# Kernel optimization log

Hardware: AMD Instinct MI355X
Metric: run time of the kernel (lower is better)

The kernel has to match this reference:

```python
import jax, jax.numpy as jnp
import numpy as np

N_STEPS = 64          # sample['N']
G = 1.0               # sample['g'] (constant diffusion)
NUM_SAMPLES = 2       # num_samples_per_obs
W_SCALE = 0.05

# interpolant coefficients: alpha(s)=1-s, beta(s)=s, sigma(s)=1-s
# derivatives: alpha_dot=-1, beta_dot=1, sigma_dot=-1

def b_net(x, x0, s, W1, b1, W2, b2, W3, b3):
    # B_net(interpolant, current_state, s): MLP on concat([x, x0, s])
    sf = jnp.full(x.shape[:-1] + (1,), s, dtype=x.dtype)
    inp = jnp.concatenate([x, x0, sf], axis=-1)      # [B, 2*dim+1]
    h = jax.nn.relu(inp @ W1 + b1)
    h = jax.nn.relu(h @ W2 + b2)
    return h @ W3 + b3                                # [B, dim]


def setup_inputs() -> dict:
    key = jax.random.key(0)
    ks = jax.random.split(key, 4)
    num_obs, dim, hid = 65536, 64, 256
    X0 = jax.random.normal(ks[0], (num_obs, dim), dtype=jnp.float32)
    W1 = jax.random.normal(ks[1], (2 * dim + 1, hid), dtype=jnp.float32) * W_SCALE
    W2 = jax.random.normal(ks[2], (hid, hid), dtype=jnp.float32) * W_SCALE
    W3 = jax.random.normal(ks[3], (hid, dim), dtype=jnp.float32) * W_SCALE
    return {
        "X0": X0,
        "W1": W1, "b1": jnp.zeros((hid,), jnp.float32),
        "W2": W2, "b2": jnp.zeros((hid,), jnp.float32),
        "W3": W3, "b3": jnp.zeros((dim,), jnp.float32),
    }


def reference(X0, W1, b1, W2, b2, W3, b3):
    time = jnp.linspace(0.0, 1.0, N_STEPS + 1, dtype=X0.dtype)
    ds = jnp.asarray(1.0 / N_STEPS, X0.dtype)
    sqrt_ds = jnp.sqrt(ds)
    params = (W1, b1, W2, b2, W3, b3)

    def sample_one(key):
        k0, kloop = jax.random.split(key)
        # first Euler step: X = X0 + ds*B(X0,X0,0) + sigma(0)*sqrt(ds)*eta
        eta0 = jax.random.normal(k0, X0.shape, X0.dtype)
        X = X0 + ds * b_net(X0, X0, time[0], *params) + (1.0 - time[0]) * sqrt_ds * eta0

        def step(carry, n):
            X, key = carry
            key, kn = jax.random.split(key)
            s = time[n]
            al, ald = 1.0 - s, -1.0
            bt, btd = s, 1.0
            sg, sgd = 1.0 - s, -1.0
            drift_b = b_net(X, X0, s, *params)
            # score correction (self.score)
            c = btd * X + (bt * ald - btd * al) * X0
            A = 1.0 / (s * sg * (btd * sg - bt * sgd))
            score = A * (bt * drift_b - c)
            # adjusted drift: drift + 0.5*(g^2 - sigma^2)*score
            control = 0.5 * (G ** 2 - sg ** 2) * score
            eta = jax.random.normal(kn, X.shape, X.dtype)
            X = X + ds * (drift_b + control) + G * sqrt_ds * eta
            return (X, key), None

        (X, _), _ = jax.lax.scan(step, (X, kloop), jnp.arange(1, N_STEPS))
        return X

    keys = jax.random.split(jax.random.key(1), NUM_SAMPLES)
    samples = jax.vmap(sample_one)(keys)   # [num_samples, num_obs, dim]
    return samples
```

## Files before the change

### kernel.cpp

```cpp
#include <hip/hip_runtime.h>
#include <stdint.h>


#define PARTITIONABLE 1

namespace {

constexpr int   kObs    = 65536;
constexpr int   kDim    = 64;
constexpr int   kSteps  = 64;
constexpr float kDs     = 1.0f / 64.0f;
constexpr float kSqrtDs = 0.125f;

constexpr int kWeightBytes = 256 * 1024;
constexpr int kKeysOff     = kWeightBytes;
constexpr int kStabOff     = kKeysOff + 1024;

typedef _Float16 f16x8 __attribute__((ext_vector_type(8)));
typedef _Float16 f16x4 __attribute__((ext_vector_type(4)));
typedef float    f32x4 __attribute__((ext_vector_type(4)));

#define MFMA16(a, b, c) __builtin_amdgcn_mfma_f32_16x16x32_f16((a), (b), (c), 0, 0, 0)

__device__ __forceinline__ uint32_t rotl(uint32_t v, int r) {
  return (v << r) | (v >> (32 - r));
}

__device__ __forceinline__ void tf2x32(uint32_t k0, uint32_t k1,
                                       uint32_t& x0, uint32_t& x1) {
  uint32_t k2 = k0 ^ k1 ^ 0x1BD11BDAu;
  x0 += k0; x1 += k1;
  x0 += x1; x1 = rotl(x1, 13); x1 ^= x0;
  x0 += x1; x1 = rotl(x1, 15); x1 ^= x0;
  x0 += x1; x1 = rotl(x1, 26); x1 ^= x0;
  x0 += x1; x1 = rotl(x1,  6); x1 ^= x0;
  x0 += k1; x1 += k2 + 1u;
  x0 += x1; x1 = rotl(x1, 17); x1 ^= x0;
  x0 += x1; x1 = rotl(x1, 29); x1 ^= x0;
  x0 += x1; x1 = rotl(x1, 16); x1 ^= x0;
  x0 += x1; x1 = rotl(x1, 24); x1 ^= x0;
  x0 += k2; x1 += k0 + 2u;
  x0 += x1; x1 = rotl(x1, 13); x1 ^= x0;
  x0 += x1; x1 = rotl(x1, 15); x1 ^= x0;
  x0 += x1; x1 = rotl(x1, 26); x1 ^= x0;
  x0 += x1; x1 = rotl(x1,  6); x1 ^= x0;
  x0 += k0; x1 += k1 + 3u;
  x0 += x1; x1 = rotl(x1, 17); x1 ^= x0;
  x0 += x1; x1 = rotl(x1, 29); x1 ^= x0;
  x0 += x1; x1 = rotl(x1, 16); x1 ^= x0;
  x0 += x1; x1 = rotl(x1, 24); x1 ^= x0;
  x0 += k1; x1 += k2 + 4u;
  x0 += x1; x1 = rotl(x1, 13); x1 ^= x0;
  x0 += x1; x1 = rotl(x1, 15); x1 ^= x0;
  x0 += x1; x1 = rotl(x1, 26); x1 ^= x0;
  x0 += x1; x1 = rotl(x1,  6); x1 ^= x0;
  x0 += k2; x1 += k0 + 5u;
}

__device__ __forceinline__ void jax_split(uint32_t k0, uint32_t k1,
                                          uint32_t& a0, uint32_t& a1,
                                          uint32_t& b0, uint32_t& b1) {
#if PARTITIONABLE
  uint32_t x0 = 0u, x1 = 0u; tf2x32(k0, k1, x0, x1); a0 = x0; a1 = x1;
  uint32_t y0 = 0u, y1 = 1u; tf2x32(k0, k1, y0, y1); b0 = y0; b1 = y1;
#else
  uint32_t x0 = 0u, x1 = 2u; tf2x32(k0, k1, x0, x1);
  uint32_t y0 = 1u, y1 = 3u; tf2x32(k0, k1, y0, y1);
  a0 = x0; a1 = y0; b0 = x1; b1 = y1;
#endif
}

__device__ __forceinline__ uint32_t draw_bits(uint32_t k0, uint32_t k1, uint32_t i) {
#if PARTITIONABLE
  uint32_t x0 = 0u, x1 = i;
  tf2x32(k0, k1, x0, x1);
  return x0 ^ x1;
#else
  const uint32_t half = (uint32_t)kObs * kDim / 2;
  if (i < half) {
    uint32_t x0 = i, x1 = i + half; tf2x32(k0, k1, x0, x1); return x0;
  } else {
    uint32_t x0 = i - half, x1 = i; tf2x32(k0, k1, x0, x1); return x1;
  }
#endif
}

__device__ __forceinline__ float erfinv32(float x) {
  float w = -__logf(fmaf(-x, x, 1.0f));
  float p;
  if (w < 5.0f) {
    w = w - 2.5f;
    p =            2.81022636e-08f;
    p = fmaf(p, w, 3.43273939e-07f);
    p = fmaf(p, w, -3.5233877e-06f);
    p = fmaf(p, w, -4.39150654e-06f);
    p = fmaf(p, w, 0.00021858087f);
    p = fmaf(p, w, -0.00125372503f);
    p = fmaf(p, w, -0.00417768164f);
    p = fmaf(p, w, 0.246640727f);
    p = fmaf(p, w, 1.50140941f);
  } else {
    w = sqrtf(w) - 3.0f;
    p =            -0.000200214257f;
    p = fmaf(p, w, 0.000100950558f);
    p = fmaf(p, w, 0.00134934322f);
    p = fmaf(p, w, -0.00367342844f);
    p = fmaf(p, w, 0.00573950773f);
    p = fmaf(p, w, -0.0076224613f);
    p = fmaf(p, w, 0.00943887047f);
    p = fmaf(p, w, 1.00167406f);
    p = fmaf(p, w, 2.83297682f);
  }
  return p * x;
}

__device__ __forceinline__ float bits_to_normal(uint32_t bits) {
  const float lo = -0.99999994f;
  float f = __uint_as_float(0x3f800000u | (bits >> 9)) - 1.0f;
  float u = fmaxf(lo, fmaf(f, 2.0f, lo));
  return 1.41421356237f * erfinv32(u);
}

}

__global__ void prep_weights(const float* __restrict__ W1,
                             const float* __restrict__ W2,
                             const float* __restrict__ W3,
                             _Float16* __restrict__ ws) {
  const int G = blockIdx.x;
  const int t = threadIdx.x;

  if (G >= 256) {
    if (t < 2) {
      uint32_t* kout = (uint32_t*)((char*)ws + kKeysOff) + t * 128;
      uint32_t s0a, s0b, s1a, s1b;
      jax_split(0u, 1u, s0a, s0b, s1a, s1b);
      const uint32_t sk0 = t ? s1a : s0a;
      const uint32_t sk1 = t ? s1b : s0b;
      uint32_t kd0, kd1, kl0, kl1;
      jax_split(sk0, sk1, kd0, kd1, kl0, kl1);
      kout[0] = kd0; kout[1] = kd1;
      for (int n = 1; n < kSteps; ++n) {
        uint32_t na, nb, xa, xb;
        jax_split(kl0, kl1, na, nb, xa, xb);
        kl0 = na; kl1 = nb;
        kout[2 * n] = xa; kout[2 * n + 1] = xb;
      }
    }
    if (t < kSteps) {
      const float s  = (float)t * kDs;
      const float sg = 1.0f - s;
      f32x4 v;
      v[0] = s;
      v[1] = (t == 0) ? 0.0f : 1.0f / (s * sg);
      v[2] = 0.5f * (1.0f - sg * sg);
      v[3] = 0.0f;
      *(f32x4*)((char*)ws + kStabOff + t * 16) = v;
    }
    return;
  }

  const int lane = t >> 2;
  const int j0   = (t & 3) * 2;
  const int w    = G >> 5;
  const int T    = G & 31;
  const int lm   = lane & 15;
  const int kb   = (lane >> 4) << 3;

#pragma unroll
  for (int jj = 0; jj < 2; ++jj) {
    const int j = j0 + jj;
    float v;
    if (T < 8) {
      const int mt = T >> 2, kt = T & 3;
      const int col = w * 32 + mt * 16 + lm;
      const int k   = kt * 32 + kb + j;
      v = W1[k * 256 + col];
    } else if (T < 24) {
      const int u = T - 8;
      const int mt = u >> 3, kt = u & 7;
      const int col = w * 32 + mt * 16 + lm;
      const int k   = kt * 32 + kb + j;
      v = W2[k * 256 + col];
    } else {
      const int kt  = T - 24;
      const int col = (w >> 1) * 16 + lm;
      const int k   = kt * 32 + kb + j;
      v = W3[k * 64 + col];
    }
    ws[(size_t)G * 512 + lane * 8 + j] = (_Float16)v;
  }
}

__global__ __launch_bounds__(512, 2)
void sde_mfma(const float* __restrict__ X0g,
              const float* __restrict__ W1,
              const float* __restrict__ b1,
              const float* __restrict__ b2,
              const float* __restrict__ b3,
              const _Float16* __restrict__ ws,
              float* __restrict__ out) {
  __shared__ alignas(16) _Float16 xA [64][72];
  __shared__ alignas(16) _Float16 x0A[64][72];
  __shared__ alignas(16) _Float16 h1 [64][264];
  __shared__ alignas(16) _Float16 h2 [64][264];
  __shared__ alignas(16) float    bb [832];

  const int t    = threadIdx.x;
  const int w    = t >> 6;
  const int l    = t & 63;
  const int lq   = l >> 4;
  const int lm   = l & 15;
  const int samp = blockIdx.x >> 10;
  const int tile = blockIdx.x & 1023;
  const int r0   = tile * 64;
  const int mt3  = w >> 1;
  const int ntb  = (w & 1) * 2;
  const int d0   = mt3 * 16 + lq * 4;

  if (t < 256) {
    bb[t]       = b1[t];
    bb[256 + t] = W1[128 * 256 + t];
    bb[512 + t] = b2[t];
  } else if (t < 320) {
    bb[768 + (t - 256)] = b3[t - 256];
  }

  {
    const int li = t >> 3;
    const int ci = (t & 7) * 8;
    const float* p = X0g + (size_t)(r0 + li) * kDim + ci;
    const float4 a = *(const float4*)p;
    const float4 b = *(const float4*)(p + 4);
    f16x8 h;
    h[0] = (_Float16)a.x; h[1] = (_Float16)a.y;
    h[2] = (_Float16)a.z; h[3] = (_Float16)a.w;
    h[4] = (_Float16)b.x; h[5] = (_Float16)b.y;
    h[6] = (_Float16)b.z; h[7] = (_Float16)b.w;
    *(f16x8*)&xA [li][ci] = h;
    *(f16x8*)&x0A[li][ci] = h;
  }

  float xv[2][4];
  f32x4 x0q[2];
#pragma unroll
  for (int ni = 0; ni < 2; ++ni) {
    const int row = (ntb + ni) * 16 + lm;
    x0q[ni] = *(const f32x4*)(X0g + (size_t)(r0 + row) * kDim + d0);
#pragma unroll
    for (int q = 0; q < 4; ++q) xv[ni][q] = x0q[ni][q];
  }

  f16x8 wreg[32];
  {
    const char* pW = (const char*)ws + (size_t)w * 32768 + l * 16;
#pragma unroll
    for (int i = 0; i < 32; ++i)
      wreg[i] = *(const f16x8*)(pW + i * 1024);
  }

  const uint32_t* keys = (const uint32_t*)((const char*)ws + kKeysOff) + samp * 128;
  const f32x4*    stab = (const f32x4*)((const char*)ws + kStabOff);

  __syncthreads();

  for (int n = 0; n < kSteps; ++n) {
    const f32x4 st = stab[n];
    const float s = st[0], A = st[1], coef = st[2];
    const uint32_t ka = keys[2 * n], kbk = keys[2 * n + 1];

#pragma unroll
    for (int nt = 0; nt < 4; ++nt) {
      const int row = nt * 16 + lm;
      f16x8 bf[4];
      bf[0] = *(const f16x8*)&xA [row][lq * 8];
      bf[1] = *(const f16x8*)&xA [row][32 + lq * 8];
      bf[2] = *(const f16x8*)&x0A[row][lq * 8];
      bf[3] = *(const f16x8*)&x0A[row][32 + lq * 8];
#pragma unroll
      for (int mt = 0; mt < 2; ++mt) {
        f32x4 c = {0.f, 0.f, 0.f, 0.f};
#pragma unroll
        for (int kt = 0; kt < 4; ++kt)
          c = MFMA16(wreg[mt * 4 + kt], bf[kt], c);
        const int nb = w * 32 + mt * 16 + lq * 4;
        const f32x4 bq = *(const f32x4*)&bb[nb];
        const f32x4 wq = *(const f32x4*)&bb[256 + nb];
        f16x4 o;
#pragma unroll
        for (int q = 0; q < 4; ++q)
          o[q] = (_Float16)fmaxf(c[q] + fmaf(s, wq[q], bq[q]), 0.f);
        *(f16x4*)&h1[row][nb] = o;
      }
    }
    __syncthreads();

#pragma unroll
    for (int ntp = 0; ntp < 2; ++ntp) {
      f32x4 c[2][2];
#pragma unroll
      for (int mt = 0; mt < 2; ++mt)
#pragma unroll
        for (int ni = 0; ni < 2; ++ni)
          c[mt][ni] = (f32x4){0.f, 0.f, 0.f, 0.f};
#pragma unroll
      for (int half = 0; half < 2; ++half) {
        f16x8 bh[2][4];
#pragma unroll
        for (int ni = 0; ni < 2; ++ni)
#pragma unroll
          for (int k4 = 0; k4 < 4; ++k4)
            bh[ni][k4] = *(const f16x8*)
                &h1[(ntp * 2 + ni) * 16 + lm][(half * 4 + k4) * 32 + lq * 8];
#pragma unroll
        for (int mt = 0; mt < 2; ++mt)
#pragma unroll
          for (int k4 = 0; k4 < 4; ++k4) {
            const f16x8 aW = wreg[8 + mt * 8 + half * 4 + k4];
            c[mt][0] = MFMA16(aW, bh[0][k4], c[mt][0]);
            c[mt][1] = MFMA16(aW, bh[1][k4], c[mt][1]);
          }
      }
#pragma unroll
      for (int mt = 0; mt < 2; ++mt) {
        const int nb = w * 32 + mt * 16 + lq * 4;
        const f32x4 bq = *(const f32x4*)&bb[512 + nb];
#pragma unroll
        for (int ni = 0; ni < 2; ++ni) {
          f16x4 o;
#pragma unroll
          for (int q = 0; q < 4; ++q)
            o[q] = (_Float16)fmaxf(c[mt][ni][q] + bq[q], 0.f);
          *(f16x4*)&h2[(ntp * 2 + ni) * 16 + lm][nb] = o;
        }
      }
    }
    __syncthreads();

    const f32x4 b3q = *(const f32x4*)&bb[768 + d0];
#pragma unroll
    for (int ni = 0; ni < 2; ++ni) {
      const int row = (ntb + ni) * 16 + lm;
      f32x4 dA = {0.f, 0.f, 0.f, 0.f}, dB = {0.f, 0.f, 0.f, 0.f};
#pragma unroll
      for (int half = 0; half < 2; ++half) {
        f16x8 bh[4];
#pragma unroll
        for (int k4 = 0; k4 < 4; ++k4)
          bh[k4] = *(const f16x8*)&h2[row][(half * 4 + k4) * 32 + lq * 8];
        dA = MFMA16(wreg[24 + half * 4 + 0], bh[0], dA);
        dB = MFMA16(wreg[24 + half * 4 + 1], bh[1], dB);
        dA = MFMA16(wreg[24 + half * 4 + 2], bh[2], dA);
        dB = MFMA16(wreg[24 + half * 4 + 3], bh[3], dB);
      }
      const uint32_t gi0 = (uint32_t)((r0 + row) * kDim + d0);
      f16x4 hx;
#pragma unroll
      for (int q = 0; q < 4; ++q) {
        const float ov    = dA[q] + dB[q] + b3q[q];
        const float eta   = bits_to_normal(draw_bits(ka, kbk, gi0 + q));
        const float score = A * (s * ov - (xv[ni][q] - x0q[ni][q]));
        const float nx    = xv[ni][q] + kDs * (ov + coef * score) + kSqrtDs * eta;
        xv[ni][q] = nx;
        hx[q] = (_Float16)nx;
      }
      *(f16x4*)&xA[row][d0] = hx;
    }
    __syncthreads();
  }

#pragma unroll
  for (int ni = 0; ni < 2; ++ni) {
    const int row = (ntb + ni) * 16 + lm;
    const size_t ob = (size_t)samp * ((size_t)kObs * kDim) +
                      (size_t)(r0 + row) * kDim + d0;
    f32x4 v;
#pragma unroll
    for (int q = 0; q < 4; ++q) v[q] = xv[ni][q];
    *(f32x4*)(out + ob) = v;
  }
}

extern "C" void kernel_launch(void* const* d_in, const int* in_sizes, int n_in,
                              void* d_out, int out_size, void* d_ws, size_t ws_size,
                              hipStream_t stream) {
  const float* X0 = (const float*)d_in[0];
  const float* W1 = (const float*)d_in[1];
  const float* b1 = (const float*)d_in[2];
  const float* W2 = (const float*)d_in[3];
  const float* b2 = (const float*)d_in[4];
  const float* W3 = (const float*)d_in[5];
  const float* b3 = (const float*)d_in[6];
  _Float16* ws = (_Float16*)d_ws;

  prep_weights<<<dim3(257), dim3(256), 0, stream>>>(W1, W2, W3, ws);
  sde_mfma<<<dim3(2048), dim3(512), 0, stream>>>(X0, W1, b1, b2, b3, ws,
                                                 (float*)d_out);
}
```

Measured before the change: 3.076 ms.

## Store LDS activations in MFMA-fragment order and hoist noise generation earlier

Replaces the padded row-major LDS arrays for x, x0, h1 and h2 with a fragment-tiled layout. In this layout each lane's MFMA operand is one contiguous 16-byte chunk at lane*16 within a 1 KB tile, which is meant to make LDS reads conflict-free and simpler to address. The Gaussian noise for the step is also computed earlier: the first half before layer 1 and the second half before the barrier that precedes layer 3. This lets the ALU-heavy RNG overlap with MFMA work instead of sitting on the critical tail. In exchange the index math is more intricate, and the precomputed noise values raise register pressure.

```diff
diff --git a/kernel.cpp b/kernel.cpp
--- a/kernel.cpp
+++ b/kernel.cpp
@@ -200,11 +200,11 @@
               const float* __restrict__ b3,
               const _Float16* __restrict__ ws,
               float* __restrict__ out) {
-  __shared__ alignas(16) _Float16 xA [64][72];
-  __shared__ alignas(16) _Float16 x0A[64][72];
-  __shared__ alignas(16) _Float16 h1 [64][264];
-  __shared__ alignas(16) _Float16 h2 [64][264];
-  __shared__ alignas(16) float    bb [832];
+  __shared__ alignas(16) char  xAf [8 * 1024];
+  __shared__ alignas(16) char  x0Af[8 * 1024];
+  __shared__ alignas(16) char  h1f [32 * 1024];
+  __shared__ alignas(16) char  h2f [32 * 1024];
+  __shared__ alignas(16) float bb  [832];
 
   const int t    = threadIdx.x;
   const int w    = t >> 6;
@@ -218,6 +218,11 @@
   const int ntb  = (w & 1) * 2;
   const int d0   = mt3 * 16 + lq * 4;
 
+  const int rb  = l * 16;
+  const int lo1 = ((lq >> 1) * 16 + lm) * 16 + (lq & 1) * 8;
+  const int kt3 = mt3 >> 1;
+  const int ln3 = (((mt3 & 1) * 2 + (lq >> 1)) * 16 + lm) * 16 + (lq & 1) * 8;
+
   if (t < 256) {
     bb[t]       = b1[t];
     bb[256 + t] = W1[128 * 256 + t];
@@ -237,8 +242,10 @@
     h[2] = (_Float16)a.z; h[3] = (_Float16)a.w;
     h[4] = (_Float16)b.x; h[5] = (_Float16)b.y;
     h[6] = (_Float16)b.z; h[7] = (_Float16)b.w;
-    *(f16x8*)&xA [li][ci] = h;
-    *(f16x8*)&x0A[li][ci] = h;
+    const int fa = ((ci >> 5) * 4 + (li >> 4)) * 1024 +
+                   (((ci >> 3) & 3) * 16 + (li & 15)) * 16;
+    *(f16x8*)(xAf  + fa) = h;
+    *(f16x8*)(x0Af + fa) = h;
   }
 
   float xv[2][4];
@@ -250,6 +257,8 @@
 #pragma unroll
     for (int q = 0; q < 4; ++q) xv[ni][q] = x0q[ni][q];
   }
+  const uint32_t giA = (uint32_t)((r0 + ntb * 16 + lm) * kDim + d0);
+  const uint32_t giB = giA + 16u * kDim;
 
   f16x8 wreg[32];
   {
@@ -269,14 +278,18 @@
     const float s = st[0], A = st[1], coef = st[2];
     const uint32_t ka = keys[2 * n], kbk = keys[2 * n + 1];
 
+    float etaA[4];
+#pragma unroll
+    for (int q = 0; q < 4; ++q)
+      etaA[q] = bits_to_normal(draw_bits(ka, kbk, giA + q));
+
 #pragma unroll
     for (int nt = 0; nt < 4; ++nt) {
-      const int row = nt * 16 + lm;
       f16x8 bf[4];
-      bf[0] = *(const f16x8*)&xA [row][lq * 8];
-      bf[1] = *(const f16x8*)&xA [row][32 + lq * 8];
-      bf[2] = *(const f16x8*)&x0A[row][lq * 8];
-      bf[3] = *(const f16x8*)&x0A[row][32 + lq * 8];
+      bf[0] = *(const f16x8*)(xAf  + (0 * 4 + nt) * 1024 + rb);
+      bf[1] = *(const f16x8*)(xAf  + (1 * 4 + nt) * 1024 + rb);
+      bf[2] = *(const f16x8*)(x0Af + (0 * 4 + nt) * 1024 + rb);
+      bf[3] = *(const f16x8*)(x0Af + (1 * 4 + nt) * 1024 + rb);
 #pragma unroll
       for (int mt = 0; mt < 2; ++mt) {
         f32x4 c = {0.f, 0.f, 0.f, 0.f};
@@ -290,7 +303,7 @@
 #pragma unroll
         for (int q = 0; q < 4; ++q)
           o[q] = (_Float16)fmaxf(c[q] + fmaf(s, wq[q], bq[q]), 0.f);
-        *(f16x4*)&h1[row][nb] = o;
+        *(f16x4*)(h1f + (w * 4 + nt) * 1024 + mt * 512 + lo1) = o;
       }
     }
     __syncthreads();
@@ -311,7 +324,7 @@
 #pragma unroll
           for (int k4 = 0; k4 < 4; ++k4)
             bh[ni][k4] = *(const f16x8*)
-                &h1[(ntp * 2 + ni) * 16 + lm][(half * 4 + k4) * 32 + lq * 8];
+                (h1f + ((half * 4 + k4) * 4 + ntp * 2 + ni) * 1024 + rb);
 #pragma unroll
         for (int mt = 0; mt < 2; ++mt)
 #pragma unroll
@@ -331,40 +344,44 @@
 #pragma unroll
           for (int q = 0; q < 4; ++q)
             o[q] = (_Float16)fmaxf(c[mt][ni][q] + bq[q], 0.f);
-          *(f16x4*)&h2[(ntp * 2 + ni) * 16 + lm][nb] = o;
+          *(f16x4*)(h2f + (w * 4 + ntp * 2 + ni) * 1024 + mt * 512 + lo1) = o;
         }
       }
     }
+
+    float etaB[4];
+#pragma unroll
+    for (int q = 0; q < 4; ++q)
+      etaB[q] = bits_to_normal(draw_bits(ka, kbk, giB + q));
     __syncthreads();
 
     const f32x4 b3q = *(const f32x4*)&bb[768 + d0];
 #pragma unroll
     for (int ni = 0; ni < 2; ++ni) {
-      const int row = (ntb + ni) * 16 + lm;
       f32x4 dA = {0.f, 0.f, 0.f, 0.f}, dB = {0.f, 0.f, 0.f, 0.f};
 #pragma unroll
       for (int half = 0; half < 2; ++half) {
         f16x8 bh[4];
 #pragma unroll
         for (int k4 = 0; k4 < 4; ++k4)
-          bh[k4] = *(const f16x8*)&h2[row][(half * 4 + k4) * 32 + lq * 8];
+          bh[k4] = *(const f16x8*)
+              (h2f + ((half * 4 + k4) * 4 + ntb + ni) * 1024 + rb);
         dA = MFMA16(wreg[24 + half * 4 + 0], bh[0], dA);
         dB = MFMA16(wreg[24 + half * 4 + 1], bh[1], dB);
         dA = MFMA16(wreg[24 + half * 4 + 2], bh[2], dA);
         dB = MFMA16(wreg[24 + half * 4 + 3], bh[3], dB);
       }
-      const uint32_t gi0 = (uint32_t)((r0 + row) * kDim + d0);
       f16x4 hx;
 #pragma unroll
       for (int q = 0; q < 4; ++q) {
         const float ov    = dA[q] + dB[q] + b3q[q];
-        const float eta   = bits_to_normal(draw_bits(ka, kbk, gi0 + q));
+        const float eta   = ni ? etaB[q] : etaA[q];
         const float score = A * (s * ov - (xv[ni][q] - x0q[ni][q]));
         const float nx    = xv[ni][q] + kDs * (ov + coef * score) + kSqrtDs * eta;
         xv[ni][q] = nx;
         hx[q] = (_Float16)nx;
       }
-      *(f16x4*)&xA[row][d0] = hx;
+      *(f16x4*)(xAf + (kt3 * 4 + ntb + ni) * 1024 + ln3) = hx;
     }
     __syncthreads();
   }
```

After: 2.934 ms. -4.6%, faster.
